# Kernel optimization log

Measured on AMD Instinct MI355X. Metric: run time of the kernel, lower is better.

The kernel has to match this reference:

```python
import jax, jax.numpy as jnp
import numpy as np

HIDDEN = 1024
D_INNER = 2048
DT_RANK = 64
STATE = 16
KCONV = 4


def setup_inputs() -> dict:
    key = jax.random.key(0)
    ks = jax.random.split(key, 9)
    s = lambda k, shape, sc=0.02: jax.random.normal(k, shape, dtype=jnp.float32) * sc
    return {
        "x": jax.random.normal(ks[0], (2, 1024, HIDDEN), dtype=jnp.float32),
        "in_proj_w": s(ks[1], (2 * D_INNER, HIDDEN)),
        "conv_w": s(ks[2], (D_INNER, 1, KCONV), 0.2),
        "conv_b": s(ks[3], (D_INNER,), 0.1),
        "x_proj_w": s(ks[4], (DT_RANK + 2 * STATE, D_INNER)),
        "dt_proj_w": s(ks[5], (D_INNER, DT_RANK), 0.1),
        "dt_proj_b": s(ks[6], (D_INNER,), 0.1),
        "A_log": s(ks[7], (D_INNER, STATE), 0.5),
        "out_proj_w": s(ks[8], (HIDDEN, D_INNER)),
    }


def _selective_scan(u, delta, A, B, C):
    # u, delta: (b,l,d); A: (d,n); B, C: (b,l,n)
    deltaA = jnp.exp(delta[..., None] * A)               # (b,l,d,n)
    dBu = (delta * u)[..., None] * B[:, :, None, :]      # (b,l,d,n)
    # scan over time axis; carry h: (b,d,n)
    deltaA_t = jnp.moveaxis(deltaA, 1, 0)                # (l,b,d,n)
    dBu_t = jnp.moveaxis(dBu, 1, 0)                      # (l,b,d,n)
    C_t = jnp.moveaxis(C, 1, 0)                          # (l,b,n)

    def step(h, inp):
        dA_i, dBu_i, C_i = inp
        h = dA_i * h + dBu_i
        y = jnp.einsum('bdn,bn->bd', h, C_i)
        return h, y

    h0 = jnp.zeros(u.shape[:1] + u.shape[2:] + (A.shape[1],), dtype=u.dtype)
    _, ys = jax.lax.scan(step, h0, (deltaA_t, dBu_t, C_t))
    return jnp.moveaxis(ys, 0, 1)                        # (b,l,d)


def reference(x, in_proj_w, conv_w, conv_b, x_proj_w, dt_proj_w, dt_proj_b, A_log, out_proj_w):
    b, l, _ = x.shape
    xr = x @ in_proj_w.T                                 # (b,l,2*d_inner)
    xs, res = jnp.split(xr, 2, axis=-1)
    # causal depthwise conv1d: pad left k-1 (matches padding=k-1 then [:l])
    xc = jnp.moveaxis(xs, 1, 2)                          # (b,d,l)
    xc = jax.lax.conv_general_dilated(
        xc, conv_w, window_strides=(1,), padding=[(KCONV - 1, 0)],
        feature_group_count=D_INNER,
        dimension_numbers=('NCH', 'OIH', 'NCH'))
    xc = xc + conv_b[None, :, None]
    xs = jnp.moveaxis(xc, 2, 1)                          # (b,l,d)
    xs = jax.nn.silu(xs)
    x_dbl = xs @ x_proj_w.T                              # (b,l,dt_rank+2n)
    dt, B, C = jnp.split(x_dbl, [DT_RANK, DT_RANK + STATE], axis=-1)
    delta = jax.nn.softplus(dt @ dt_proj_w.T + dt_proj_b)
    A = -jnp.exp(A_log.astype(jnp.float32))
    y = _selective_scan(xs, delta, A, B, C)
    y = y * jax.nn.silu(res)
    return y @ out_proj_w.T
```

## Files before the change

### kernel.cpp

```cpp
#include <hip/hip_runtime.h>

typedef unsigned short u16;
typedef __bf16 bf16x8 __attribute__((ext_vector_type(8)));
typedef float f32x4 __attribute__((ext_vector_type(4)));

__device__ inline float bf2f(u16 u) {
    unsigned int x = ((unsigned int)u) << 16;
    return __builtin_bit_cast(float, x);
}
__device__ inline u16 f2bf(float f) {
    unsigned int x = __builtin_bit_cast(unsigned int, f);
    return (u16)((x + 0x7FFFu + ((x >> 16) & 1u)) >> 16);
}
__device__ inline float sigm(float v) { return 1.f / (1.f + __expf(-v)); }

__device__ inline uint4 pack8(const float* p) {
    const float4* q = (const float4*)p;
    float4 a = q[0], b = q[1];
    union { u16 h[8]; uint4 v; } u;
    u.h[0] = f2bf(a.x); u.h[1] = f2bf(a.y); u.h[2] = f2bf(a.z); u.h[3] = f2bf(a.w);
    u.h[4] = f2bf(b.x); u.h[5] = f2bf(b.y); u.h[6] = f2bf(b.z); u.h[7] = f2bf(b.w);
    return u.v;
}

__global__ __launch_bounds__(256)
void cvt_bf16(const float* __restrict__ in, u16* __restrict__ out)
{
    int i = blockIdx.x * 256 + threadIdx.x;
    ((uint4*)out)[i] = pack8(in + (size_t)i * 8);
}
__global__ __launch_bounds__(256)
void cvt_pad_xproj(const float* __restrict__ in, u16* __restrict__ out)
{
    int i = blockIdx.x * 256 + threadIdx.x;
    int row = (i * 8) >> 11;
    ((uint4*)out)[i] = (row < 96) ? pack8(in + (size_t)row * 2048 + ((i * 8) & 2047))
                                  : make_uint4(0u, 0u, 0u, 0u);
}

template<int EPI, bool OUTF32>
__global__ __launch_bounds__(256, 2)
void gemm2(const u16* __restrict__ A, int lda,
           const u16* __restrict__ B, int ldb,
           void* __restrict__ Cout, int ldc,
           int N, int ksplit, size_t zElems,
           const float* __restrict__ bias)
{
    __shared__ u16 sA[128][40];
    __shared__ u16 sB[128][40];

    const int tid  = threadIdx.x;
    const int lane = tid & 63;
    const int wave = tid >> 6;
    const int wm = (wave >> 1) * 64;
    const int wn = (wave & 1) * 64;
    const int m0 = blockIdx.y * 128;
    const int n0 = blockIdx.x * 128;
    const int lm = lane & 15;
    const int kq = (lane >> 4) * 8;
    const int k0 = blockIdx.z * ksplit;

    const int r0 = tid >> 2, q0 = (tid & 3) * 8;
    const int r1 = (tid + 256) >> 2, q1 = ((tid + 256) & 3) * 8;
    const u16* gA0 = A + (size_t)(m0 + r0) * lda + k0 + q0;
    const u16* gA1 = A + (size_t)(m0 + r1) * lda + k0 + q1;
    const u16* gB0 = B + (size_t)(n0 + r0) * ldb + k0 + q0;
    const u16* gB1 = B + (size_t)(n0 + r1) * ldb + k0 + q1;

    f32x4 acc[4][4] = {};

    uint4 pa0 = *(const uint4*)gA0, pa1 = *(const uint4*)gA1;
    uint4 pb0 = *(const uint4*)gB0, pb1 = *(const uint4*)gB1;

    for (int kb = 0; kb < ksplit; kb += 32) {
        *(uint4*)&sA[r0][q0] = pa0;
        *(uint4*)&sA[r1][q1] = pa1;
        *(uint4*)&sB[r0][q0] = pb0;
        *(uint4*)&sB[r1][q1] = pb1;
        __syncthreads();

        if (kb + 32 < ksplit) {
            pa0 = *(const uint4*)(gA0 + kb + 32);
            pa1 = *(const uint4*)(gA1 + kb + 32);
            pb0 = *(const uint4*)(gB0 + kb + 32);
            pb1 = *(const uint4*)(gB1 + kb + 32);
        }

        bf16x8 af[4], bfr[4];
        #pragma unroll
        for (int i = 0; i < 4; ++i)
            af[i] = *(const bf16x8*)&sA[wm + i * 16 + lm][kq];
        #pragma unroll
        for (int j = 0; j < 4; ++j)
            bfr[j] = *(const bf16x8*)&sB[wn + j * 16 + lm][kq];
        #pragma unroll
        for (int i = 0; i < 4; ++i)
            #pragma unroll
            for (int j = 0; j < 4; ++j)
                acc[i][j] = __builtin_amdgcn_mfma_f32_16x16x32_bf16(af[i], bfr[j], acc[i][j], 0, 0, 0);
        __syncthreads();
    }

    #pragma unroll
    for (int i = 0; i < 4; ++i) {
        int crow = m0 + wm + i * 16 + ((lane >> 4) << 2);
        #pragma unroll
        for (int j = 0; j < 4; ++j) {
            int ccol = n0 + wn + j * 16 + lm;
            if (ccol < N) {
                #pragma unroll
                for (int r = 0; r < 4; ++r) {
                    float v = acc[i][j][r];
                    if (EPI == 2 && ccol >= 2048) v *= sigm(v);
                    size_t off = (size_t)blockIdx.z * zElems + (size_t)(crow + r) * ldc + ccol;
                    if (OUTF32) ((float*)Cout)[off] = v;
                    else        ((u16*)Cout)[off]   = f2bf(v);
                }
            }
        }
    }
}

__global__ __launch_bounds__(256)
void dt_delta(const u16* __restrict__ xdbl, const float* __restrict__ dtw,
              const float* __restrict__ bias, u16* __restrict__ out)
{
    const int tid = threadIdx.x;
    const int d   = blockIdx.x * 256 + tid;
    const int t0  = blockIdx.y * 16;

    __shared__ float s_x[16][64];

    if (tid < 128) {
        int tok = tid >> 3, ch = tid & 7;
        uint4 v = *(const uint4*)&xdbl[(size_t)(t0 + tok) * 96 + ch * 8];
        const u16* h = (const u16*)&v;
        #pragma unroll
        for (int e = 0; e < 8; ++e) s_x[tok][ch * 8 + e] = bf2f(h[e]);
    }

    float w[64];
    {
        const float4* wp = (const float4*)(dtw + (size_t)d * 64);
        #pragma unroll
        for (int q = 0; q < 16; ++q) {
            float4 v = wp[q];
            w[q * 4 + 0] = v.x; w[q * 4 + 1] = v.y;
            w[q * 4 + 2] = v.z; w[q * 4 + 3] = v.w;
        }
    }
    const float bd = bias[d];
    __syncthreads();

    for (int tok = 0; tok < 16; ++tok) {
        float a0 = bd, a1 = 0.f, a2 = 0.f, a3 = 0.f;
        const float4* xv4 = (const float4*)s_x[tok];
        #pragma unroll
        for (int q = 0; q < 16; ++q) {
            float4 xv = xv4[q];
            a0 = fmaf(w[q * 4 + 0], xv.x, a0);
            a1 = fmaf(w[q * 4 + 1], xv.y, a1);
            a2 = fmaf(w[q * 4 + 2], xv.z, a2);
            a3 = fmaf(w[q * 4 + 3], xv.w, a3);
        }
        float v = (a0 + a1) + (a2 + a3);
        v = (v > 20.f) ? v : log1pf(__expf(v));
        out[(size_t)(t0 + tok) * 4096 + d] = f2bf(v);
    }
}

__global__ __launch_bounds__(256)
void reduce96(const float* __restrict__ splits, u16* __restrict__ xdbl)
{
    int i = blockIdx.x * 256 + threadIdx.x;
    float acc = 0.f;
    #pragma unroll
    for (int z = 0; z < 8; ++z) acc += splits[(size_t)z * 196608 + i];
    xdbl[i] = f2bf(acc);
}

__global__ __launch_bounds__(256)
void reduce_out(const u16* __restrict__ parts, float* __restrict__ out)
{
    int i = blockIdx.x * 256 + threadIdx.x;
    float acc[8] = {};
    #pragma unroll
    for (int z = 0; z < 4; ++z) {
        uint4 v = ((const uint4*)(parts + (size_t)z * 2097152))[i];
        const u16* h = (const u16*)&v;
        #pragma unroll
        for (int e = 0; e < 8; ++e) acc[e] += bf2f(h[e]);
    }
    float4* o = (float4*)(out + (size_t)i * 8);
    o[0] = make_float4(acc[0], acc[1], acc[2], acc[3]);
    o[1] = make_float4(acc[4], acc[5], acc[6], acc[7]);
}

__global__ __launch_bounds__(256)
void conv_silu(const u16* __restrict__ xr, const float* __restrict__ w,
               const float* __restrict__ bias, u16* __restrict__ xs)
{
    int idx = blockIdx.x * 256 + threadIdx.x;
    int d = idx & 2047, t = (idx >> 11) & 1023, b = idx >> 21;
    const u16* base = xr + (size_t)b * 1024 * 4096;
    float acc = bias[d];
    #pragma unroll
    for (int j = 0; j < 4; ++j) {
        int ti = t - 3 + j;
        if (ti >= 0) acc = fmaf(w[d * 4 + j], bf2f(base[(size_t)ti * 4096 + d]), acc);
    }
    xs[idx] = f2bf(acc * sigm(acc));
}

template<int PHC>
__global__ __launch_bounds__(256)
void scan_chunk(const u16* __restrict__ deltag, u16* __restrict__ xsg,
                const u16* __restrict__ xdbl, const float* __restrict__ A_log,
                const u16* __restrict__ xr, float* __restrict__ summ,
                float* __restrict__ ssum)
{
    const int tid = threadIdx.x;
    const int d0 = blockIdx.x * 256;
    const int c  = blockIdx.y;
    const int b  = blockIdx.z;
    const int d  = d0 + tid;
    const int tok0 = b * 1024 + c * 32;

    __shared__ u16 s_del[32][256];
    __shared__ u16 s_uu[32][256];
    __shared__ u16 s_bc[32][32];
    __shared__ u16 s_res[PHC ? 32 : 1][PHC ? 256 : 1];
    __shared__ u16 s_y[PHC ? 32 : 1][PHC ? 256 : 1];

    for (int i = tid; i < 1024; i += 256) {
        int tl = i >> 5, v = i & 31;
        size_t tok = (size_t)(tok0 + tl);
        *(uint4*)&s_del[tl][v * 8] = *(const uint4*)&deltag[tok * 4096 + d0 + v * 8];
        *(uint4*)&s_uu[tl][v * 8]  = *(const uint4*)&xsg[tok * 2048 + d0 + v * 8];
        if (PHC)
            *(uint4*)&s_res[tl][v * 8] = *(const uint4*)&xr[tok * 4096 + 2048 + d0 + v * 8];
    }
    for (int i = tid; i < 1024; i += 256) {
        int tl = i >> 5, j = i & 31;
        s_bc[tl][j] = xdbl[(size_t)(tok0 + tl) * 96 + 64 + j];
    }

    float Ar[16], h[16];
    {
        const float4* Ap = (const float4*)(A_log + (size_t)d * 16);
        #pragma unroll
        for (int q = 0; q < 4; ++q) {
            float4 a = Ap[q];
            Ar[q * 4 + 0] = -__expf(a.x); Ar[q * 4 + 1] = -__expf(a.y);
            Ar[q * 4 + 2] = -__expf(a.z); Ar[q * 4 + 3] = -__expf(a.w);
        }
    }
    if (PHC) {
        const float4* hp = (const float4*)&summ[((size_t)(b * 32 + c) * 2048 + d) * 16];
        #pragma unroll
        for (int q = 0; q < 4; ++q) {
            float4 v = hp[q];
            h[q * 4 + 0] = v.x; h[q * 4 + 1] = v.y; h[q * 4 + 2] = v.z; h[q * 4 + 3] = v.w;
        }
    } else {
        #pragma unroll
        for (int n = 0; n < 16; ++n) h[n] = 0.f;
    }
    __syncthreads();

    float S = 0.f;
    #pragma unroll 4
    for (int tl = 0; tl < 32; ++tl) {
        float dlt = bf2f(s_del[tl][tid]);
        float du = dlt * bf2f(s_uu[tl][tid]);
        if (!PHC) S += dlt;
        #pragma unroll
        for (int n = 0; n < 16; ++n)
            h[n] = fmaf(__expf(dlt * Ar[n]), h[n], du * bf2f(s_bc[tl][n]));
        if (PHC) {
            float y = 0.f;
            #pragma unroll
            for (int n = 0; n < 16; ++n)
                y = fmaf(h[n], bf2f(s_bc[tl][16 + n]), y);
            s_y[tl][tid] = f2bf(y * bf2f(s_res[tl][tid]));
        }
    }

    if (!PHC) {
        float4* bp = (float4*)&summ[((size_t)(b * 32 + c) * 2048 + d) * 16];
        #pragma unroll
        for (int q = 0; q < 4; ++q)
            bp[q] = make_float4(h[q * 4], h[q * 4 + 1], h[q * 4 + 2], h[q * 4 + 3]);
        ssum[(size_t)(b * 32 + c) * 2048 + d] = S;
    } else {
        __syncthreads();
        for (int i = tid; i < 1024; i += 256) {
            int tl = i >> 5, v = i & 31;
            *(uint4*)&xsg[(size_t)(tok0 + tl) * 2048 + d0 + v * 8] = *(uint4*)&s_y[tl][v * 8];
        }
    }
}

__global__ __launch_bounds__(256)
void scan_phaseB(float* __restrict__ summ, const float* __restrict__ ssum,
                 const float* __restrict__ A_log)
{
    int g = blockIdx.x * 256 + threadIdx.x;
    int n = g & 15;
    int d = (g >> 4) & 2047;
    int b = g >> 15;
    float An = -__expf(A_log[(size_t)d * 16 + n]);
    float h = 0.f;
    for (int c = 0; c < 32; ++c) {
        size_t idx = ((size_t)(b * 32 + c) * 2048 + d) * 16 + n;
        float bc = summ[idx];
        float Sc = ssum[(size_t)(b * 32 + c) * 2048 + d];
        summ[idx] = h;
        h = fmaf(__expf(An * Sc), h, bc);
    }
}

__global__ void sentinel_kernel(float* out, float v) { out[0] = v; }

extern "C" void kernel_launch(void* const* d_in, const int* in_sizes, int n_in,
                              void* d_out, int out_size, void* d_ws, size_t ws_size,
                              hipStream_t stream)
{
    const float* x         = (const float*)d_in[0];
    const float* in_w      = (const float*)d_in[1];
    const float* conv_w    = (const float*)d_in[2];
    const float* conv_b    = (const float*)d_in[3];
    const float* xproj_w   = (const float*)d_in[4];
    const float* dtproj_w  = (const float*)d_in[5];
    const float* dtproj_b  = (const float*)d_in[6];
    const float* A_log     = (const float*)d_in[7];
    const float* outproj_w = (const float*)d_in[8];
    float* out = (float*)d_out;

    static const int EXP[9] = {2097152, 4194304, 8192, 2048, 196608, 131072, 2048, 32768, 2097152};
    int bad = -1;
    if (n_in != 9) bad = 9;
    else { for (int i = 0; i < 9; ++i) if (in_sizes[i] != EXP[i]) { bad = i; break; } }
    if (bad < 0 && out_size != 2097152) bad = 10;
    if (bad < 0 && ws_size < 34734080u) bad = 11;
    if (bad >= 0) {
        sentinel_kernel<<<1, 1, 0, stream>>>(out, 131072.f * (1.f + (float)bad / 16.f));
        return;
    }

    char* ws = (char*)d_ws;
    u16*   xr      = (u16*)(ws);
    u16*   xs      = (u16*)(ws + 16777216);
    u16*   xdbl    = (u16*)(ws + 25165824);
    char*  R       = ws + 25559040;
    u16*   x_bf    = xs;
    u16*   inw_bf  = (u16*)(R);
    u16*   xpw_bf  = (u16*)(R + 8388608);
    float* splits  = (float*)(R);
    float* summ    = (float*)(R);
    float* ssum    = (float*)(R + 8388608);
    u16*   opw_bf  = (u16*)(R);
    u16*   oparts  = xr;

    cvt_bf16<<<1024, 256, 0, stream>>>(x, x_bf);
    cvt_bf16<<<2048, 256, 0, stream>>>(in_w, inw_bf);
    cvt_pad_xproj<<<128, 256, 0, stream>>>(xproj_w, xpw_bf);
    gemm2<2, false><<<dim3(32, 16, 1), 256, 0, stream>>>(
        x_bf, 1024, inw_bf, 1024, xr, 4096, 4096, 1024, 0, nullptr);
    conv_silu<<<16384, 256, 0, stream>>>(xr, conv_w, conv_b, xs);
    gemm2<0, true><<<dim3(1, 16, 8), 256, 0, stream>>>(
        xs, 2048, xpw_bf, 2048, splits, 96, 96, 256, 196608, nullptr);
    reduce96<<<768, 256, 0, stream>>>(splits, xdbl);
    dt_delta<<<dim3(8, 128), 256, 0, stream>>>(xdbl, dtproj_w, dtproj_b, xr);
    scan_chunk<0><<<dim3(8, 32, 2), 256, 0, stream>>>(xr, xs, xdbl, A_log, xr, summ, ssum);
    scan_phaseB<<<256, 256, 0, stream>>>(summ, ssum, A_log);
    scan_chunk<1><<<dim3(8, 32, 2), 256, 0, stream>>>(xr, xs, xdbl, A_log, xr, summ, ssum);
    cvt_bf16<<<1024, 256, 0, stream>>>(outproj_w, opw_bf);
    gemm2<0, false><<<dim3(8, 16, 4), 256, 0, stream>>>(
        xs, 2048, opw_bf, 2048, oparts, 1024, 1024, 512, 2097152, nullptr);
    reduce_out<<<1024, 256, 0, stream>>>(oparts, out);
}
```

Measured before the change: 264.7 us.

## Load GEMM tiles directly to LDS with XOR swizzle and BK=64

After: 260.6 us. About the same (-1.6%).

```diff
diff --git a/kernel.cpp b/kernel.cpp
--- a/kernel.cpp
+++ b/kernel.cpp
@@ -13,6 +13,12 @@
     return (u16)((x + 0x7FFFu + ((x >> 16) & 1u)) >> 16);
 }
 __device__ inline float sigm(float v) { return 1.f / (1.f + __expf(-v)); }
+
+__device__ __forceinline__ void gload16(const void* g, void* l) {
+    __builtin_amdgcn_global_load_lds(
+        (const __attribute__((address_space(1))) void*)g,
+        (__attribute__((address_space(3))) void*)l, 16, 0, 0);
+}
 
 __device__ inline uint4 pack8(const float* p) {
     const float4* q = (const float4*)p;
@@ -46,8 +52,8 @@
            int N, int ksplit, size_t zElems,
            const float* __restrict__ bias)
 {
-    __shared__ u16 sA[128][40];
-    __shared__ u16 sB[128][40];
+    __shared__ u16 sA[128][64];
+    __shared__ u16 sB[128][64];
 
     const int tid  = threadIdx.x;
     const int lane = tid & 63;
@@ -57,47 +63,45 @@
     const int m0 = blockIdx.y * 128;
     const int n0 = blockIdx.x * 128;
     const int lm = lane & 15;
-    const int kq = (lane >> 4) * 8;
+    const int g  = lane >> 4;
     const int k0 = blockIdx.z * ksplit;
 
-    const int r0 = tid >> 2, q0 = (tid & 3) * 8;
-    const int r1 = (tid + 256) >> 2, q1 = ((tid + 256) & 3) * 8;
-    const u16* gA0 = A + (size_t)(m0 + r0) * lda + k0 + q0;
-    const u16* gA1 = A + (size_t)(m0 + r1) * lda + k0 + q1;
-    const u16* gB0 = B + (size_t)(n0 + r0) * ldb + k0 + q0;
-    const u16* gB1 = B + (size_t)(n0 + r1) * ldb + k0 + q1;
+    const int rr = lane >> 3;
+    const int sl = lane & 7;
+    const int xsl = sl ^ rr;
+    const u16* gA = A + (size_t)(m0 + wave * 8 + rr) * lda + k0 + xsl * 8;
+    const u16* gB = B + (size_t)(n0 + wave * 8 + rr) * ldb + k0 + xsl * 8;
+    const int ldsRow = (wave * 8) * 128;
 
     f32x4 acc[4][4] = {};
 
-    uint4 pa0 = *(const uint4*)gA0, pa1 = *(const uint4*)gA1;
-    uint4 pb0 = *(const uint4*)gB0, pb1 = *(const uint4*)gB1;
-
-    for (int kb = 0; kb < ksplit; kb += 32) {
-        *(uint4*)&sA[r0][q0] = pa0;
-        *(uint4*)&sA[r1][q1] = pa1;
-        *(uint4*)&sB[r0][q0] = pb0;
-        *(uint4*)&sB[r1][q1] = pb1;
+    for (int kb = 0; kb < ksplit; kb += 64) {
+        #pragma unroll
+        for (int c = 0; c < 4; ++c) {
+            gload16(gA + (size_t)c * 32 * lda + kb, (char*)sA + c * 4096 + ldsRow);
+            gload16(gB + (size_t)c * 32 * ldb + kb, (char*)sB + c * 4096 + ldsRow);
+        }
         __syncthreads();
 
-        if (kb + 32 < ksplit) {
-            pa0 = *(const uint4*)(gA0 + kb + 32);
-            pa1 = *(const uint4*)(gA1 + kb + 32);
-            pb0 = *(const uint4*)(gB0 + kb + 32);
-            pb1 = *(const uint4*)(gB1 + kb + 32);
-        }
-
-        bf16x8 af[4], bfr[4];
-        #pragma unroll
-        for (int i = 0; i < 4; ++i)
-            af[i] = *(const bf16x8*)&sA[wm + i * 16 + lm][kq];
-        #pragma unroll
-        for (int j = 0; j < 4; ++j)
-            bfr[j] = *(const bf16x8*)&sB[wn + j * 16 + lm][kq];
-        #pragma unroll
-        for (int i = 0; i < 4; ++i)
+        bf16x8 af[2][4], bfr[2][4];
+        #pragma unroll
+        for (int h = 0; h < 2; ++h) {
             #pragma unroll
-            for (int j = 0; j < 4; ++j)
-                acc[i][j] = __builtin_amdgcn_mfma_f32_16x16x32_bf16(af[i], bfr[j], acc[i][j], 0, 0, 0);
+            for (int i = 0; i < 4; ++i) {
+                int ra = wm + i * 16 + lm;
+                int rb = wn + i * 16 + lm;
+                int chunk = (((h << 2) | g) ^ (lm & 7)) << 4;
+                af[h][i]  = *(const bf16x8*)((const char*)sA + ra * 128 + chunk);
+                bfr[h][i] = *(const bf16x8*)((const char*)sB + rb * 128 + chunk);
+            }
+        }
+        #pragma unroll
+        for (int h = 0; h < 2; ++h)
+            #pragma unroll
+            for (int i = 0; i < 4; ++i)
+                #pragma unroll
+                for (int j = 0; j < 4; ++j)
+                    acc[i][j] = __builtin_amdgcn_mfma_f32_16x16x32_bf16(af[h][i], bfr[h][j], acc[i][j], 0, 0, 0);
         __syncthreads();
     }
 
```
